# Kernel tuning notes

Hardware: AMD Instinct MI355X
Metric: run time of the kernel (lower is better)

Reference implementation:

```python
import jax, jax.numpy as jnp
import numpy as np
import math

FACTOR = 5

def setup_inputs() -> dict:
    key = jax.random.key(0)
    k1, k2, k3, k4 = jax.random.split(key, 4)
    B, L, H, D = 2, 4096, 8, 64
    sample_k = min(FACTOR * int(np.ceil(np.log(L))), L)  # 45
    return {
        "queries": jax.random.normal(k1, (B, L, H, D), dtype=jnp.float32),
        "keys": jax.random.normal(k2, (B, L, H, D), dtype=jnp.float32),
        "values": jax.random.normal(k3, (B, L, H, D), dtype=jnp.float32),
        "attn_mask": jnp.zeros((1,), dtype=bool),  # unused (mask_flag=False)
        "index_sample": jax.random.randint(k4, (L, sample_k), 0, L, dtype=jnp.int64),
    }

def reference(queries, keys, values, attn_mask, index_sample):
    B, L_Q, H, D = queries.shape
    L_K = keys.shape[1]
    # [B,L,H,D] -> [B,H,L,D]
    q = jnp.transpose(queries, (0, 2, 1, 3))
    k = jnp.transpose(keys, (0, 2, 1, 3))
    v = jnp.transpose(values, (0, 2, 1, 3))

    n_top = min(FACTOR * int(np.ceil(np.log(L_Q))), L_Q)  # u

    # --- _prob_QK ---
    # K_sample[b,h,l,s,e] = k[b,h,index_sample[l,s],e]
    K_sample = k[:, :, index_sample, :]                      # [B,H,L_Q,S,E]
    Q_K_sample = jnp.einsum('bhle,bhlse->bhls', q, K_sample)  # [B,H,L_Q,S]
    # sparsity measure: max - mean(over full L_K as in torch code)
    M = Q_K_sample.max(axis=-1) - Q_K_sample.sum(axis=-1) / L_K  # [B,H,L_Q]
    M_top = jax.lax.top_k(M, n_top)[1]                        # [B,H,u] indices

    Q_reduce = jnp.take_along_axis(q, M_top[..., None], axis=2)  # [B,H,u,E]
    scores_top = jnp.einsum('bhue,bhke->bhuk', Q_reduce, k)      # [B,H,u,L_K]

    scale = 1.0 / math.sqrt(D)
    attn = jax.nn.softmax(scale * scores_top, axis=-1)           # [B,H,u,L_K]
    context_in_q = jnp.einsum('bhuk,bhkd->bhud', attn, v)        # [B,H,u,D]

    # scatter selected contexts into zero-initialized tensor
    b_idx = jnp.arange(B)[:, None, None]
    h_idx = jnp.arange(H)[None, :, None]
    context = jnp.zeros((B, H, L_Q, D), dtype=queries.dtype)
    context = context.at[b_idx, h_idx, M_top].set(context_in_q)

    return jnp.transpose(context, (0, 2, 1, 3))  # [B,L_Q,H,D]
```

## Files before the change

kernel.cpp:

```cpp
#include <hip/hip_runtime.h>
#include <math.h>

#define B_ 2
#define L_ 4096
#define H_ 8
#define D_ 64
#define S_ 45
#define NTOP_ 45
#define SCALE 0.125f
#define TKEYS 128

__global__ __launch_bounds__(256) void compute_M_kernel(
    const float* __restrict__ q, const float* __restrict__ k,
    const int* __restrict__ samp, float* __restrict__ M) {
    __shared__ int sIdx[32 * S_];
    int tid = threadIdx.x;
    int g   = blockIdx.x;
    int xcd = g & 7;
    int s0  = g >> 3;
    int bh  = xcd + 8 * (s0 >> 7);
    int c32 = s0 & 127;
    int b = bh >> 3, h = bh & 7;
    int l0 = c32 * 32;

    const int* sbase = samp + (long)l0 * S_;
    for (int i = tid; i < 32 * S_; i += 256) sIdx[i] = sbase[i];
    __syncthreads();

    int lane = tid & 63, wave = tid >> 6;
    int l8 = lane & 7;
    int q8 = lane >> 3;
    int qi = wave * 8 + q8;
    int l  = l0 + qi;

    const float4* qrow = (const float4*)(q + (((long)(b * L_ + l)) * H_ + h) * D_);
    float4 qa = qrow[l8], qb = qrow[8 + l8];

    const float4* kb4 = (const float4*)(k + ((long)b * L_ * H_ + h) * (long)D_);
    const int* myIdx = sIdx + qi * S_;

    int idx0 = myIdx[0];
    const float4* kr0 = kb4 + (long)idx0 * (H_ * D_ / 4);
    float4 ka = kr0[l8], kb2 = kr0[8 + l8];

    float vmax = -INFINITY, vsum = 0.f;
    #pragma unroll 5
    for (int s = 0; s < S_; ++s) {
        int sn = (s + 1 < S_) ? s + 1 : s;
        int nidx = myIdx[sn];
        const float4* nr = kb4 + (long)nidx * (H_ * D_ / 4);
        float4 na = nr[l8], nb = nr[8 + l8];

        float p = qa.x * ka.x + qa.y * ka.y + qa.z * ka.z + qa.w * ka.w
                + qb.x * kb2.x + qb.y * kb2.y + qb.z * kb2.z + qb.w * kb2.w;
        p += __shfl_xor(p, 1, 64);
        p += __shfl_xor(p, 2, 64);
        p += __shfl_xor(p, 4, 64);
        vmax = fmaxf(vmax, p);
        vsum += p;

        ka = na; kb2 = nb;
    }
    if (l8 == 0) M[(long)bh * L_ + l] = vmax - vsum * (1.0f / (float)L_);
}

__global__ __launch_bounds__(256) void topk_kernel(
    const float* __restrict__ M, int* __restrict__ topIdx) {
    __shared__ unsigned int hist[256];
    __shared__ unsigned int suf[257];
    __shared__ unsigned int wsum[4];
    __shared__ int sBin, sRemain, sCnt, sTieCnt;
    __shared__ int tie[64];

    int bh = blockIdx.x, tid = threadIdx.x;
    int lane = tid & 63, wave = tid >> 6;
    const float* row = M + (long)bh * L_;

    unsigned int key[16];
    #pragma unroll
    for (int j = 0; j < 16; ++j) {
        unsigned int bts = __float_as_uint(row[tid + 256 * j]);
        key[j] = bts ^ ((unsigned int)((int)bts >> 31) | 0x80000000u);
    }

    unsigned int prefix = 0, pmask = 0;
    int remain = NTOP_;
    #pragma unroll 1
    for (int pass = 3; pass >= 0; --pass) {
        int shift = pass * 8;
        hist[tid] = 0;
        __syncthreads();
        #pragma unroll
        for (int j = 0; j < 16; ++j) {
            if ((key[j] & pmask) == prefix)
                atomicAdd(&hist[(key[j] >> shift) & 255u], 1u);
        }
        __syncthreads();
        unsigned int s = hist[tid];
        #pragma unroll
        for (int off = 1; off < 64; off <<= 1) {
            unsigned int o = __shfl_down(s, off, 64);
            if (lane + off < 64) s += o;
        }
        if (lane == 0) wsum[wave] = s;
        __syncthreads();
        unsigned int add = 0;
        for (int w = wave + 1; w < 4; ++w) add += wsum[w];
        s += add;
        suf[tid] = s;
        if (tid == 0) suf[256] = 0;
        __syncthreads();
        if (suf[tid] >= (unsigned int)remain && suf[tid + 1] < (unsigned int)remain) {
            sBin = tid;
            sRemain = remain - (int)suf[tid + 1];
        }
        __syncthreads();
        prefix |= ((unsigned int)sBin) << shift;
        pmask  |= 0xFFu << shift;
        remain  = sRemain;
        __syncthreads();
    }

    if (tid == 0) { sCnt = 0; sTieCnt = 0; }
    __syncthreads();
    int* outRow = topIdx + bh * NTOP_;
    #pragma unroll
    for (int j = 0; j < 16; ++j) {
        int idx = tid + 256 * j;
        if (key[j] > prefix) {
            int pos = atomicAdd(&sCnt, 1);
            outRow[pos] = idx;
        } else if (key[j] == prefix) {
            int tp = atomicAdd(&sTieCnt, 1);
            if (tp < 64) tie[tp] = idx;
        }
    }
    __syncthreads();
    if (tid == 0) {
        int base = sCnt;
        int tc = sTieCnt < 64 ? sTieCnt : 64;
        for (int t = 0; t < remain; ++t) {
            int mi = 0x7fffffff, mj = 0;
            for (int j2 = 0; j2 < tc; ++j2)
                if (tie[j2] < mi) { mi = tie[j2]; mj = j2; }
            outRow[base + t] = mi;
            tie[mj] = 0x7fffffff;
        }
    }
}

#define QSTRIDE 68
#define PSTRIDE 132
__global__ __launch_bounds__(256, 2) void attn_strip_kernel(
    const float* __restrict__ q, const float* __restrict__ k,
    const float* __restrict__ v, const int* __restrict__ topIdx,
    float* __restrict__ pOut, float* __restrict__ plPart,
    int nsplit, int ntiles) {
    __shared__ int   sTop[48];
    __shared__ float sQ[48 * QSTRIDE];
    __shared__ float sKV[TKEYS * QSTRIDE];
    __shared__ float sP[48 * PSTRIDE];

    int g = blockIdx.x;
    int xcd = g & 7;
    int s0 = g >> 3;
    int grp = s0 / nsplit;
    int bh = xcd + 8 * grp;
    int split = s0 - grp * nsplit;
    int b = bh >> 3, h = bh & 7;
    int tid = threadIdx.x;

    if (tid < 48) sTop[tid] = (tid < NTOP_) ? topIdx[bh * NTOP_ + tid] : 0;
    __syncthreads();

    for (int i = tid; i < 768; i += 256) {
        int u = i >> 4, d4 = i & 15;
        float4 val = make_float4(0.f, 0.f, 0.f, 0.f);
        if (u < NTOP_) {
            int lq = sTop[u];
            val = *(const float4*)(q + (((long)(b * L_ + lq)) * H_ + h) * D_ + 4 * d4);
        }
        *(float4*)(sQ + u * QSTRIDE + 4 * d4) = val;
    }

    int tx = tid & 15, ty = tid >> 4;
    int dx = tid & 15, uy = tid >> 4;
    float o[3][4];
    float ls[3];
    #pragma unroll
    for (int i = 0; i < 3; ++i) {
        ls[i] = 0.f;
        #pragma unroll
        for (int c = 0; c < 4; ++c) o[i][c] = 0.f;
    }

    #pragma unroll 1
    for (int tile = 0; tile < ntiles; ++tile) {
        int key0 = (split * ntiles + tile) * TKEYS;
        __syncthreads();
        #pragma unroll
        for (int j = 0; j < 8; ++j) {
            int i = tid + 256 * j;
            int r = i >> 4, d4 = i & 15;
            float4 val = *(const float4*)(k + (((long)(b * L_ + key0 + r)) * H_ + h) * D_ + 4 * d4);
            *(float4*)(sKV + r * QSTRIDE + 4 * d4) = val;
        }
        __syncthreads();

        float acc[3][8];
        #pragma unroll
        for (int i = 0; i < 3; ++i)
            #pragma unroll
            for (int j = 0; j < 8; ++j) acc[i][j] = 0.f;

        #pragma unroll 4
        for (int d4 = 0; d4 < 16; ++d4) {
            float4 qv[3];
            #pragma unroll
            for (int i = 0; i < 3; ++i)
                qv[i] = *(const float4*)(sQ + (3 * ty + i) * QSTRIDE + 4 * d4);
            #pragma unroll
            for (int j = 0; j < 8; ++j) {
                float4 kv = *(const float4*)(sKV + (tx + 16 * j) * QSTRIDE + 4 * d4);
                #pragma unroll
                for (int i = 0; i < 3; ++i)
                    acc[i][j] += qv[i].x * kv.x + qv[i].y * kv.y + qv[i].z * kv.z + qv[i].w * kv.w;
            }
        }
        #pragma unroll
        for (int i = 0; i < 3; ++i) {
            #pragma unroll
            for (int j = 0; j < 8; ++j)
                sP[(3 * ty + i) * PSTRIDE + tx + 16 * j] = __expf(acc[i][j] * SCALE);
        }
        __syncthreads();

        #pragma unroll
        for (int j = 0; j < 8; ++j) {
            int i = tid + 256 * j;
            int r = i >> 4, d4 = i & 15;
            float4 val = *(const float4*)(v + (((long)(b * L_ + key0 + r)) * H_ + h) * D_ + 4 * d4);
            *(float4*)(sKV + r * QSTRIDE + 4 * d4) = val;
        }
        __syncthreads();

        #pragma unroll 2
        for (int k4 = 0; k4 < 32; ++k4) {
            float pa[3][4];
            #pragma unroll
            for (int i = 0; i < 3; ++i)
                *(float4*)pa[i] = *(const float4*)(sP + (3 * uy + i) * PSTRIDE + 4 * k4);
            #pragma unroll
            for (int c = 0; c < 4; ++c) {
                float4 vr = *(const float4*)(sKV + (4 * k4 + c) * QSTRIDE + 4 * dx);
                #pragma unroll
                for (int i = 0; i < 3; ++i) {
                    o[i][0] += pa[i][c] * vr.x;
                    o[i][1] += pa[i][c] * vr.y;
                    o[i][2] += pa[i][c] * vr.z;
                    o[i][3] += pa[i][c] * vr.w;
                    ls[i]   += pa[i][c];
                }
            }
        }
    }

    #pragma unroll
    for (int i = 0; i < 3; ++i) {
        int u = 3 * uy + i;
        if (u < NTOP_) {
            long base = ((long)(split * 16 + bh) * NTOP_ + u) * D_;
            *(float4*)(pOut + base + 4 * dx) = make_float4(o[i][0], o[i][1], o[i][2], o[i][3]);
            if (dx == 0) plPart[(long)(split * 16 + bh) * NTOP_ + u] = ls[i];
        }
    }
}

__global__ __launch_bounds__(64) void reduce_norm_kernel(
    const int* __restrict__ topIdx, const float* __restrict__ pOut,
    const float* __restrict__ plPart, float* __restrict__ out, int nsplit) {
    int u = blockIdx.x, bh = blockIdx.y;
    int b = bh >> 3, h = bh & 7;
    int d = threadIdx.x;
    float acc = 0.f, lsum = 0.f;
    for (int s = 0; s < nsplit; ++s) {
        acc  += pOut[((long)(s * 16 + bh) * NTOP_ + u) * D_ + d];
        lsum += plPart[(long)(s * 16 + bh) * NTOP_ + u];
    }
    int lq = topIdx[bh * NTOP_ + u];
    out[(((long)(b * L_ + lq)) * H_ + h) * D_ + d] = acc / lsum;
}

extern "C" void kernel_launch(void* const* d_in, const int* in_sizes, int n_in,
                              void* d_out, int out_size, void* d_ws, size_t ws_size,
                              hipStream_t stream) {
    const float* q = (const float*)d_in[0];
    const float* k = (const float*)d_in[1];
    const float* v = (const float*)d_in[2];
    const int* samp = (const int*)d_in[4];
    float* out = (float*)d_out;

    char* ws = (char*)d_ws;
    const size_t mBytes   = (size_t)B_ * H_ * L_ * sizeof(float);
    const size_t topBytes = (size_t)B_ * H_ * NTOP_ * sizeof(int);
    const size_t plBytes  = (size_t)32 * 16 * NTOP_ * sizeof(float);
    float* M      = (float*)ws;
    int*   topIdx = (int*)(ws + mBytes);
    float* plPart = (float*)(ws + mBytes + topBytes);
    float* pOut   = (float*)(ws + mBytes + topBytes + plBytes);

    int nsplit = 32;
    while (nsplit > 1) {
        size_t need = mBytes + topBytes + plBytes +
                      (size_t)nsplit * 16 * NTOP_ * D_ * sizeof(float);
        if (need <= ws_size) break;
        nsplit >>= 1;
    }
    int ntiles = 32 / nsplit;

    hipMemsetAsync(d_out, 0, (size_t)out_size * sizeof(float), stream);

    compute_M_kernel<<<2048, 256, 0, stream>>>(q, k, samp, M);

    topk_kernel<<<B_ * H_, 256, 0, stream>>>(M, topIdx);

    attn_strip_kernel<<<nsplit * B_ * H_, 256, 0, stream>>>(
        q, k, v, topIdx, pOut, plPart, nsplit, ntiles);

    dim3 gn(NTOP_, B_ * H_);
    reduce_norm_kernel<<<gn, 64, 0, stream>>>(topIdx, pOut, plPart, out, nsplit);
}
```

Measured before the change: 162.5 us.

## Split attention into single-tile blocks, deepen M prefetch, parallelize split reduction

After: 158.9 us. 1.02x faster.

```diff
diff --git a/kernel.cpp b/kernel.cpp
--- a/kernel.cpp
+++ b/kernel.cpp
@@ -8,12 +8,13 @@
 #define S_ 45
 #define NTOP_ 45
 #define SCALE 0.125f
-#define TKEYS 128
+#define TKEYS 64
+#define NSPLIT 64
 
 __global__ __launch_bounds__(256) void compute_M_kernel(
     const float* __restrict__ q, const float* __restrict__ k,
     const int* __restrict__ samp, float* __restrict__ M) {
-    __shared__ int sIdx[32 * S_];
+    __shared__ int sIdx[32 * 48];
     int tid = threadIdx.x;
     int g   = blockIdx.x;
     int xcd = g & 7;
@@ -24,7 +25,11 @@
     int l0 = c32 * 32;
 
     const int* sbase = samp + (long)l0 * S_;
-    for (int i = tid; i < 32 * S_; i += 256) sIdx[i] = sbase[i];
+    for (int i = tid; i < 32 * S_; i += 256) {
+        int qq = i / S_, ss = i - qq * S_;
+        sIdx[qq * 48 + ss] = sbase[i];
+    }
+    if (tid < 96) sIdx[(tid >> 2) * 48 + S_ + (tid & 3) % 3] = 0;
     __syncthreads();
 
     int lane = tid & 63, wave = tid >> 6;
@@ -37,29 +42,30 @@
     float4 qa = qrow[l8], qb = qrow[8 + l8];
 
     const float4* kb4 = (const float4*)(k + ((long)b * L_ * H_ + h) * (long)D_);
-    const int* myIdx = sIdx + qi * S_;
-
-    int idx0 = myIdx[0];
-    const float4* kr0 = kb4 + (long)idx0 * (H_ * D_ / 4);
-    float4 ka = kr0[l8], kb2 = kr0[8 + l8];
+    const int* myIdx = sIdx + qi * 48;
+
+    const float4* r0 = kb4 + (long)myIdx[0] * (H_ * D_ / 4);
+    float4 ka0 = r0[l8], kb0 = r0[8 + l8];
+    const float4* r1 = kb4 + (long)myIdx[1] * (H_ * D_ / 4);
+    float4 ka1 = r1[l8], kb1 = r1[8 + l8];
 
     float vmax = -INFINITY, vsum = 0.f;
-    #pragma unroll 5
+    #pragma unroll 3
     for (int s = 0; s < S_; ++s) {
-        int sn = (s + 1 < S_) ? s + 1 : s;
-        int nidx = myIdx[sn];
+        int nidx = myIdx[s + 2];
         const float4* nr = kb4 + (long)nidx * (H_ * D_ / 4);
         float4 na = nr[l8], nb = nr[8 + l8];
 
-        float p = qa.x * ka.x + qa.y * ka.y + qa.z * ka.z + qa.w * ka.w
-                + qb.x * kb2.x + qb.y * kb2.y + qb.z * kb2.z + qb.w * kb2.w;
+        float p = qa.x * ka0.x + qa.y * ka0.y + qa.z * ka0.z + qa.w * ka0.w
+                + qb.x * kb0.x + qb.y * kb0.y + qb.z * kb0.z + qb.w * kb0.w;
         p += __shfl_xor(p, 1, 64);
         p += __shfl_xor(p, 2, 64);
         p += __shfl_xor(p, 4, 64);
         vmax = fmaxf(vmax, p);
         vsum += p;
 
-        ka = na; kb2 = nb;
+        ka0 = ka1; kb0 = kb1;
+        ka1 = na;  kb1 = nb;
     }
     if (l8 == 0) M[(long)bh * L_ + l] = vmax - vsum * (1.0f / (float)L_);
 }
@@ -149,17 +155,15 @@
     }
 }
 
-#define QSTRIDE 68
-#define PSTRIDE 132
+#define STRIDE 68
 __global__ __launch_bounds__(256, 2) void attn_strip_kernel(
     const float* __restrict__ q, const float* __restrict__ k,
     const float* __restrict__ v, const int* __restrict__ topIdx,
-    float* __restrict__ pOut, float* __restrict__ plPart,
-    int nsplit, int ntiles) {
-    __shared__ int   sTop[48];
-    __shared__ float sQ[48 * QSTRIDE];
-    __shared__ float sKV[TKEYS * QSTRIDE];
-    __shared__ float sP[48 * PSTRIDE];
+    float* __restrict__ pOut, float* __restrict__ plPart, int nsplit) {
+    __shared__ float sQ[48 * STRIDE];
+    __shared__ float sK[TKEYS * STRIDE];
+    __shared__ float sV[TKEYS * STRIDE];
+    __shared__ float sP[48 * STRIDE];
 
     int g = blockIdx.x;
     int xcd = g & 7;
@@ -169,21 +173,58 @@
     int split = s0 - grp * nsplit;
     int b = bh >> 3, h = bh & 7;
     int tid = threadIdx.x;
-
-    if (tid < 48) sTop[tid] = (tid < NTOP_) ? topIdx[bh * NTOP_ + tid] : 0;
-    __syncthreads();
-
-    for (int i = tid; i < 768; i += 256) {
+    int key0 = split * TKEYS;
+
+    #pragma unroll
+    for (int j = 0; j < 3; ++j) {
+        int i = tid + 256 * j;
         int u = i >> 4, d4 = i & 15;
         float4 val = make_float4(0.f, 0.f, 0.f, 0.f);
         if (u < NTOP_) {
-            int lq = sTop[u];
+            int lq = topIdx[bh * NTOP_ + u];
             val = *(const float4*)(q + (((long)(b * L_ + lq)) * H_ + h) * D_ + 4 * d4);
         }
-        *(float4*)(sQ + u * QSTRIDE + 4 * d4) = val;
-    }
+        *(float4*)(sQ + u * STRIDE + 4 * d4) = val;
+    }
+    #pragma unroll
+    for (int j = 0; j < 4; ++j) {
+        int i = tid + 256 * j;
+        int r = i >> 4, d4 = i & 15;
+        long off = (((long)(b * L_ + key0 + r)) * H_ + h) * D_ + 4 * d4;
+        *(float4*)(sK + r * STRIDE + 4 * d4) = *(const float4*)(k + off);
+        *(float4*)(sV + r * STRIDE + 4 * d4) = *(const float4*)(v + off);
+    }
+    __syncthreads();
 
     int tx = tid & 15, ty = tid >> 4;
+    float acc[3][4];
+    #pragma unroll
+    for (int i = 0; i < 3; ++i)
+        #pragma unroll
+        for (int j = 0; j < 4; ++j) acc[i][j] = 0.f;
+
+    #pragma unroll 4
+    for (int d4 = 0; d4 < 16; ++d4) {
+        float4 qv[3];
+        #pragma unroll
+        for (int i = 0; i < 3; ++i)
+            qv[i] = *(const float4*)(sQ + (3 * ty + i) * STRIDE + 4 * d4);
+        #pragma unroll
+        for (int j = 0; j < 4; ++j) {
+            float4 kv = *(const float4*)(sK + (tx + 16 * j) * STRIDE + 4 * d4);
+            #pragma unroll
+            for (int i = 0; i < 3; ++i)
+                acc[i][j] += qv[i].x * kv.x + qv[i].y * kv.y + qv[i].z * kv.z + qv[i].w * kv.w;
+        }
+    }
+    #pragma unroll
+    for (int i = 0; i < 3; ++i) {
+        #pragma unroll
+        for (int j = 0; j < 4; ++j)
+            sP[(3 * ty + i) * STRIDE + tx + 16 * j] = __expf(acc[i][j] * SCALE);
+    }
+    __syncthreads();
+
     int dx = tid & 15, uy = tid >> 4;
     float o[3][4];
     float ls[3];
@@ -193,78 +234,25 @@
         #pragma unroll
         for (int c = 0; c < 4; ++c) o[i][c] = 0.f;
     }
-
-    #pragma unroll 1
-    for (int tile = 0; tile < ntiles; ++tile) {
-        int key0 = (split * ntiles + tile) * TKEYS;
-        __syncthreads();
-        #pragma unroll
-        for (int j = 0; j < 8; ++j) {
-            int i = tid + 256 * j;
-            int r = i >> 4, d4 = i & 15;
-            float4 val = *(const float4*)(k + (((long)(b * L_ + key0 + r)) * H_ + h) * D_ + 4 * d4);
-            *(float4*)(sKV + r * QSTRIDE + 4 * d4) = val;
-        }
-        __syncthreads();
-
-        float acc[3][8];
+    #pragma unroll 4
+    for (int k4 = 0; k4 < 16; ++k4) {
+        float pa[3][4];
         #pragma unroll
         for (int i = 0; i < 3; ++i)
+            *(float4*)pa[i] = *(const float4*)(sP + (3 * uy + i) * STRIDE + 4 * k4);
+        #pragma unroll
+        for (int c = 0; c < 4; ++c) {
+            float4 vr = *(const float4*)(sV + (4 * k4 + c) * STRIDE + 4 * dx);
             #pragma unroll
-            for (int j = 0; j < 8; ++j) acc[i][j] = 0.f;
-
-        #pragma unroll 4
-        for (int d4 = 0; d4 < 16; ++d4) {
-            float4 qv[3];
-            #pragma unroll
-            for (int i = 0; i < 3; ++i)
-                qv[i] = *(const float4*)(sQ + (3 * ty + i) * QSTRIDE + 4 * d4);
-            #pragma unroll
-            for (int j = 0; j < 8; ++j) {
-                float4 kv = *(const float4*)(sKV + (tx + 16 * j) * QSTRIDE + 4 * d4);
-                #pragma unroll
-                for (int i = 0; i < 3; ++i)
-                    acc[i][j] += qv[i].x * kv.x + qv[i].y * kv.y + qv[i].z * kv.z + qv[i].w * kv.w;
+            for (int i = 0; i < 3; ++i) {
+                o[i][0] += pa[i][c] * vr.x;
+                o[i][1] += pa[i][c] * vr.y;
+                o[i][2] += pa[i][c] * vr.z;
+                o[i][3] += pa[i][c] * vr.w;
+                ls[i]   += pa[i][c];
             }
         }
-        #pragma unroll
-        for (int i = 0; i < 3; ++i) {
-            #pragma unroll
-            for (int j = 0; j < 8; ++j)
-                sP[(3 * ty + i) * PSTRIDE + tx + 16 * j] = __expf(acc[i][j] * SCALE);
-        }
-        __syncthreads();
-
-        #pragma unroll
-        for (int j = 0; j < 8; ++j) {
-            int i = tid + 256 * j;
-            int r = i >> 4, d4 = i & 15;
-            float4 val = *(const float4*)(v + (((long)(b * L_ + key0 + r)) * H_ + h) * D_ + 4 * d4);
-            *(float4*)(sKV + r * QSTRIDE + 4 * d4) = val;
-        }
-        __syncthreads();
-
-        #pragma unroll 2
-        for (int k4 = 0; k4 < 32; ++k4) {
-            float pa[3][4];
-            #pragma unroll
-            for (int i = 0; i < 3; ++i)
-                *(float4*)pa[i] = *(const float4*)(sP + (3 * uy + i) * PSTRIDE + 4 * k4);
-            #pragma unroll
-            for (int c = 0; c < 4; ++c) {
-                float4 vr = *(const float4*)(sKV + (4 * k4 + c) * QSTRIDE + 4 * dx);
-                #pragma unroll
-                for (int i = 0; i < 3; ++i) {
-                    o[i][0] += pa[i][c] * vr.x;
-                    o[i][1] += pa[i][c] * vr.y;
-                    o[i][2] += pa[i][c] * vr.z;
-                    o[i][3] += pa[i][c] * vr.w;
-                    ls[i]   += pa[i][c];
-                }
-            }
-        }
-    }
-
+    }
     #pragma unroll
     for (int i = 0; i < 3; ++i) {
         int u = 3 * uy + i;
@@ -276,19 +264,29 @@
     }
 }
 
-__global__ __launch_bounds__(64) void reduce_norm_kernel(
+__global__ __launch_bounds__(256) void reduce_norm_kernel(
     const int* __restrict__ topIdx, const float* __restrict__ pOut,
     const float* __restrict__ plPart, float* __restrict__ out, int nsplit) {
+    __shared__ float part[4][64];
+    __shared__ float lpart[4];
     int u = blockIdx.x, bh = blockIdx.y;
     int b = bh >> 3, h = bh & 7;
-    int d = threadIdx.x;
+    int tid = threadIdx.x;
+    int d = tid & 63, sg = tid >> 6;
     float acc = 0.f, lsum = 0.f;
-    for (int s = 0; s < nsplit; ++s) {
+    for (int s = sg; s < nsplit; s += 4) {
         acc  += pOut[((long)(s * 16 + bh) * NTOP_ + u) * D_ + d];
         lsum += plPart[(long)(s * 16 + bh) * NTOP_ + u];
     }
-    int lq = topIdx[bh * NTOP_ + u];
-    out[(((long)(b * L_ + lq)) * H_ + h) * D_ + d] = acc / lsum;
+    part[sg][d] = acc;
+    if (d == 0) lpart[sg] = lsum;
+    __syncthreads();
+    if (sg == 0) {
+        float a = part[0][d] + part[1][d] + part[2][d] + part[3][d];
+        float lt = lpart[0] + lpart[1] + lpart[2] + lpart[3];
+        int lq = topIdx[bh * NTOP_ + u];
+        out[(((long)(b * L_ + lq)) * H_ + h) * D_ + d] = a / lt;
+    }
 }
 
 extern "C" void kernel_launch(void* const* d_in, const int* in_sizes, int n_in,
@@ -303,20 +301,19 @@
     char* ws = (char*)d_ws;
     const size_t mBytes   = (size_t)B_ * H_ * L_ * sizeof(float);
     const size_t topBytes = (size_t)B_ * H_ * NTOP_ * sizeof(int);
-    const size_t plBytes  = (size_t)32 * 16 * NTOP_ * sizeof(float);
+    const size_t plBytes  = (size_t)NSPLIT * 16 * NTOP_ * sizeof(float);
     float* M      = (float*)ws;
     int*   topIdx = (int*)(ws + mBytes);
     float* plPart = (float*)(ws + mBytes + topBytes);
     float* pOut   = (float*)(ws + mBytes + topBytes + plBytes);
 
-    int nsplit = 32;
+    int nsplit = NSPLIT;
     while (nsplit > 1) {
         size_t need = mBytes + topBytes + plBytes +
                       (size_t)nsplit * 16 * NTOP_ * D_ * sizeof(float);
         if (need <= ws_size) break;
         nsplit >>= 1;
     }
-    int ntiles = 32 / nsplit;
 
     hipMemsetAsync(d_out, 0, (size_t)out_size * sizeof(float), stream);
 
@@ -325,8 +322,8 @@
     topk_kernel<<<B_ * H_, 256, 0, stream>>>(M, topIdx);
 
     attn_strip_kernel<<<nsplit * B_ * H_, 256, 0, stream>>>(
-        q, k, v, topIdx, pOut, plPart, nsplit, ntiles);
+        q, k, v, topIdx, pOut, plPart, nsplit);
 
     dim3 gn(NTOP_, B_ * H_);
-    reduce_norm_kernel<<<gn, 64, 0, stream>>>(topIdx, pOut, plPart, out, nsplit);
-}
+    reduce_norm_kernel<<<gn, 256, 0, stream>>>(topIdx, pOut, plPart, out, nsplit);
+}
```
